# Optimization experiments

Measured on AMD Instinct MI355X. Metric: run time of the kernel, lower is better.

## Reference

```python
import jax, jax.numpy as jnp
import numpy as np

EPS = 1e-3  # keras LayerNormalization default epsilon


def layer_norm(x, gamma, beta):
    mu = jnp.mean(x, axis=-1, keepdims=True)
    var = jnp.var(x, axis=-1, keepdims=True)
    return (x - mu) * jax.lax.rsqrt(var + EPS) * gamma + beta


def setup_inputs() -> dict:
    key = jax.random.key(0)
    ks = jax.random.split(key, 16)
    B, S, D = 8, 2048, 1024          # batch, seq, input_size
    P = 2 * D                        # up-projection dim (proj_factor=2)
    H = 1024                         # hidden = head_size(64) * num_heads(16)
    s = 0.02
    inp = {
        "x": jax.random.normal(ks[0], (B, S, D), jnp.float32),
        "ln1_g": jnp.ones((D,), jnp.float32),
        "ln1_b": jnp.zeros((D,), jnp.float32),
        "W_up": jax.random.normal(ks[1], (D, P), jnp.float32) * s,
        "b_up": jnp.zeros((P,), jnp.float32),
        "W_adj": jax.random.normal(ks[2], (P, H), jnp.float32) * s,
        "b_adj": jnp.zeros((H,), jnp.float32),
        "W_q": jax.random.normal(ks[3], (H, H), jnp.float32) * s,
        "b_q": jnp.zeros((H,), jnp.float32),
        "W_k": jax.random.normal(ks[4], (H, H), jnp.float32) * s,
        "b_k": jnp.zeros((H,), jnp.float32),
        "W_v": jax.random.normal(ks[5], (H, H), jnp.float32) * s,
        "b_v": jnp.zeros((H,), jnp.float32),
        "W_i": jax.random.normal(ks[6], (H, H), jnp.float32) * s,
        "b_i": jnp.zeros((H,), jnp.float32),
        "W_f": jax.random.normal(ks[7], (H, H), jnp.float32) * s,
        "b_f": jnp.zeros((H,), jnp.float32),
        "W_o": jax.random.normal(ks[8], (H, H), jnp.float32) * s,
        "b_o": jnp.zeros((H,), jnp.float32),
        "ln2_g": jnp.ones((H,), jnp.float32),
        "ln2_b": jnpos if False else jnp.zeros((H,), jnp.float32),
        "W_down": jax.random.normal(ks[9], (H, D), jnp.float32) * s,
        "b_down": jnp.zeros((D,), jnp.float32),
    }
    return inp


def reference(x, ln1_g, ln1_b, W_up, b_up, W_adj, b_adj,
              W_q, b_q, W_k, b_k, W_v, b_v,
              W_i, b_i, W_f, b_f, W_o, b_o,
              ln2_g, ln2_b, W_down, b_down):
    head_size = 64
    x_norm = layer_norm(x, ln1_g, ln1_b)
    x_up = x_norm @ W_up + b_up                      # [B,S,2D]
    x_adj = x_up @ W_adj + b_adj                     # [B,S,H]
    # BlockDiagonal layers: each block is a Dense over the FULL input,
    # concatenated -> equivalent to one [H,H] matmul with concatenated weights.
    q = x_adj @ W_q + b_q
    k = (x_adj @ W_k + b_k) / (head_size ** 0.5)
    v = x_adj @ W_v + b_v
    i_t = x_adj @ W_i + b_i
    f_t = x_adj @ W_f + b_f
    o = jax.nn.sigmoid(x_adj @ W_o + b_o)
    m_t = jnp.maximum(f_t, i_t)
    f = jnp.exp(f_t - m_t)                           # (i = exp(i_t - m_t) unused downstream)
    c_t = f * v * k
    h_t = o * (c_t * q) / jnp.maximum(jnp.abs(k * q), 1.0)
    out = layer_norm(h_t, ln2_g, ln2_b) * jax.nn.sigmoid(x_adj)
    out = out @ W_down + b_down
    return out + x
```

## Files before the change

kernel.cpp:

```cpp
#include <hip/hip_runtime.h>


typedef unsigned short u16;
typedef __attribute__((ext_vector_type(4))) unsigned short u16x4;
typedef __attribute__((ext_vector_type(8))) __bf16 bf16x8;
typedef __attribute__((ext_vector_type(4))) float f32x4;

__device__ __forceinline__ float bf2f(u16 u) {
    union { unsigned int i; float f; } c; c.i = ((unsigned int)u) << 16; return c.f;
}
__device__ __forceinline__ u16 f2bf(float f) {
    union { float f; unsigned int i; } c; c.f = f;
    unsigned int lsb = (c.i >> 16) & 1u;
    c.i += 0x7fffu + lsb;
    return (u16)(c.i >> 16);
}
__device__ __forceinline__ float sigmoidf(float z) {
    return 1.0f / (1.0f + __expf(-z));
}

#define GLDS16(gp, lp)                                                        \
    __builtin_amdgcn_global_load_lds(                                         \
        (__attribute__((address_space(1))) void*)(void*)(gp),                 \
        (__attribute__((address_space(3))) void*)(lp), 16, 0, 0)

#define BM 128
#define BN 128
#define BK 32

template <int MODE>
__global__ __launch_bounds__(256) void gemm_bt(
    const u16* __restrict__ A, const u16* __restrict__ Bt,
    const float* __restrict__ bias, const float* __restrict__ resid,
    void* __restrict__ out, int M, int N, int K, float scale)
{
    __shared__ __align__(16) u16 As[2 * BM * BK];
    __shared__ __align__(16) u16 Bs[2 * BN * BK];

    const int tid  = threadIdx.x;
    const int lane = tid & 63;
    const int wave = tid >> 6;
    const int l15  = lane & 15;
    const int quad = lane >> 4;

    const long bm = (long)blockIdx.y * BM;
    const long bn = (long)blockIdx.x * BN;
    const int  wm = (wave >> 1) * 64;
    const int  wn = (wave & 1) * 64;

    f32x4 acc[4][4] = {};

    const int  r0 = tid >> 2;
    const int  ck = (((tid & 3) ^ ((tid >> 3) & 3)) * 8);
    const u16* ga0 = A  + (bm + r0) * (long)K + ck;
    const u16* gb0 = Bt + (bn + r0) * (long)K + ck;
    const int  ldst = wave * 512;

    auto stage = [&](int t_, int b_) {
        const long kof = (long)t_ * BK;
        u16* dA = &As[b_ * (BM * BK) + ldst];
        u16* dB = &Bs[b_ * (BN * BK) + ldst];
        GLDS16(ga0 + kof, dA);
        GLDS16(ga0 + kof + 64 * (long)K, dA + 2048);
        GLDS16(gb0 + kof, dB);
        GLDS16(gb0 + kof + 64 * (long)K, dB + 2048);
    };

    const int q8s = (quad ^ ((l15 >> 1) & 3)) * 8;
    const int nk  = K / BK;

    stage(0, 0);
    stage(1, 1);

    for (int t = 0; t < nk; ++t) {
        const int cur = t & 1;
        if (t + 1 < nk) asm volatile("s_waitcnt vmcnt(4)" ::: "memory");
        else            asm volatile("s_waitcnt vmcnt(0)" ::: "memory");
        __builtin_amdgcn_s_barrier();

        bf16x8 af[4], bfr[4];
#pragma unroll
        for (int t4 = 0; t4 < 4; ++t4) {
            af[t4]  = *(const bf16x8*)&As[cur * (BM * BK) + (wm + t4 * 16 + l15) * BK + q8s];
            bfr[t4] = *(const bf16x8*)&Bs[cur * (BN * BK) + (wn + t4 * 16 + l15) * BK + q8s];
        }
        asm volatile("s_waitcnt lgkmcnt(0)" ::: "memory");
        __builtin_amdgcn_s_barrier();
        if (t + 2 < nk) stage(t + 2, cur);

#pragma unroll
        for (int mt = 0; mt < 4; ++mt)
#pragma unroll
            for (int nt = 0; nt < 4; ++nt)
                acc[mt][nt] = __builtin_amdgcn_mfma_f32_16x16x32_bf16(
                    af[mt], bfr[nt], acc[mt][nt], 0, 0, 0);
    }

#pragma unroll
    for (int nt = 0; nt < 4; ++nt) {
        const long n  = bn + wn + nt * 16 + l15;
        const float bv = bias[n];
#pragma unroll
        for (int mt = 0; mt < 4; ++mt) {
            const long m0 = bm + wm + mt * 16 + quad * 4;
#pragma unroll
            for (int r = 0; r < 4; ++r) {
                const long idx = (m0 + r) * N + n;
                const float val = (acc[mt][nt][r] + bv) * scale;
                if (MODE == 0) ((u16*)out)[idx] = f2bf(val);
                else           ((float*)out)[idx] = val + resid[idx];
            }
        }
    }
}

__global__ __launch_bounds__(256) void gemm_gates(
    const u16* __restrict__ A, const u16* __restrict__ Wcat,
    const float* __restrict__ bq_, const float* __restrict__ bk_,
    const float* __restrict__ bv_, const float* __restrict__ bi_,
    const float* __restrict__ bf_, const float* __restrict__ bo_,
    u16* __restrict__ ht, int M, int N, int K)
{
    __shared__ __align__(16) u16 As[2 * 128 * 64];
    __shared__ __align__(16) u16 Bs[2 * 6 * 32 * 64];

    const int tid  = threadIdx.x;
    const int lane = tid & 63;
    const int wave = tid >> 6;
    const int l15  = lane & 15;
    const int quad = lane >> 4;

    const long bm = (long)blockIdx.y * 128;
    const long bn = (long)blockIdx.x * 32;

    f32x4 acc[6][4] = {};

    const int  rr = lane >> 3;
    const int  ck = (((lane & 7) ^ rr) * 8);

    const u16* gaj[4];
    int lAo[4];
#pragma unroll
    for (int j = 0; j < 4; ++j) {
        const int c = wave * 4 + j;
        gaj[j] = A + (bm + c * 8 + rr) * (long)K + ck;
        lAo[j] = c * 512;
    }
    const u16* gbj[6];
    int lBo[6];
#pragma unroll
    for (int j = 0; j < 6; ++j) {
        const int c = wave * 6 + j;
        const int g = c >> 2;
        const int r = (c & 3) * 8 + rr;
        gbj[j] = Wcat + ((long)g * 1024 + bn + r) * (long)K + ck;
        lBo[j] = c * 512;
    }

    auto stage = [&](int t_, int b_) {
        const long kof = (long)t_ * 64;
#pragma unroll
        for (int j = 0; j < 4; ++j)
            GLDS16(gaj[j] + kof, &As[b_ * 8192 + lAo[j]]);
#pragma unroll
        for (int j = 0; j < 6; ++j)
            GLDS16(gbj[j] + kof, &Bs[b_ * 12288 + lBo[j]]);
    };

    const int mh = (wave >> 1) * 64;
    const int nb = (wave & 1) * 16;
    const int l7 = l15 & 7;
    const int nk = K >> 6;

    stage(0, 0);
    stage(1, 1);

    for (int t = 0; t < nk; ++t) {
        const int cur = t & 1;
        if (t + 1 < nk) asm volatile("s_waitcnt vmcnt(10)" ::: "memory");
        else            asm volatile("s_waitcnt vmcnt(0)"  ::: "memory");
        __builtin_amdgcn_s_barrier();

        const int ab = cur * 8192;
        const int bb = cur * 12288;

        {
            const int so = (quad ^ l7) * 8;
            bf16x8 af[4];
#pragma unroll
            for (int t4 = 0; t4 < 4; ++t4)
                af[t4] = *(const bf16x8*)&As[ab + (mh + t4 * 16 + l15) * 64 + so];
#pragma unroll
            for (int g = 0; g < 6; ++g) {
                const bf16x8 bfrag =
                    *(const bf16x8*)&Bs[bb + (g * 32 + nb + l15) * 64 + so];
#pragma unroll
                for (int t4 = 0; t4 < 4; ++t4)
                    acc[g][t4] = __builtin_amdgcn_mfma_f32_16x16x32_bf16(
                        af[t4], bfrag, acc[g][t4], 0, 0, 0);
            }
        }
        bf16x8 af1[4], bf1[6];
        {
            const int so = ((4 + quad) ^ l7) * 8;
#pragma unroll
            for (int t4 = 0; t4 < 4; ++t4)
                af1[t4] = *(const bf16x8*)&As[ab + (mh + t4 * 16 + l15) * 64 + so];
#pragma unroll
            for (int g = 0; g < 6; ++g)
                bf1[g] = *(const bf16x8*)&Bs[bb + (g * 32 + nb + l15) * 64 + so];
        }
        asm volatile("s_waitcnt lgkmcnt(0)" ::: "memory");
        __builtin_amdgcn_s_barrier();
        if (t + 2 < nk) stage(t + 2, cur);

#pragma unroll
        for (int g = 0; g < 6; ++g)
#pragma unroll
            for (int t4 = 0; t4 < 4; ++t4)
                acc[g][t4] = __builtin_amdgcn_mfma_f32_16x16x32_bf16(
                    af1[t4], bf1[g], acc[g][t4], 0, 0, 0);
    }

    const long n = bn + nb + l15;
    const float bqn = bq_[n], bkn = bk_[n], bvn = bv_[n];
    const float bin = bi_[n], bfn = bf_[n], bon = bo_[n];
#pragma unroll
    for (int t = 0; t < 4; ++t) {
        const long m0 = bm + mh + t * 16 + quad * 4;
#pragma unroll
        for (int r = 0; r < 4; ++r) {
            const float qf = acc[0][t][r] + bqn;
            const float kf = (acc[1][t][r] + bkn) * 0.125f;
            const float vf = acc[2][t][r] + bvn;
            const float fi = acc[3][t][r] + bin;
            const float ff = acc[4][t][r] + bfn;
            const float osig = sigmoidf(acc[5][t][r] + bon);
            const float mx = fmaxf(ff, fi);
            const float fe = __expf(ff - mx);
            const float ct = fe * vf * kf;
            const float h  = osig * (ct * qf) / fmaxf(fabsf(kf * qf), 1.0f);
            ht[(m0 + r) * N + n] = f2bf(h);
        }
    }
}

__global__ __launch_bounds__(256) void ln_in_kernel(
    const float* __restrict__ x, const float* __restrict__ g,
    const float* __restrict__ b, u16* __restrict__ xn)
{
    const long row = blockIdx.x;
    const int  tid = threadIdx.x;
    const float4 v = ((const float4*)(x + row * 1024))[tid];
    float s  = v.x + v.y + v.z + v.w;
    float s2 = v.x * v.x + v.y * v.y + v.z * v.z + v.w * v.w;
#pragma unroll
    for (int off = 32; off > 0; off >>= 1) {
        s  += __shfl_down(s, off);
        s2 += __shfl_down(s2, off);
    }
    __shared__ float red[8];
    const int wave = tid >> 6;
    if ((tid & 63) == 0) { red[wave] = s; red[4 + wave] = s2; }
    __syncthreads();
    if (tid == 0) {
        const float S  = red[0] + red[1] + red[2] + red[3];
        const float S2 = red[4] + red[5] + red[6] + red[7];
        const float mu = S * (1.0f / 1024.0f);
        const float var = S2 * (1.0f / 1024.0f) - mu * mu;
        red[0] = mu; red[1] = rsqrtf(var + 1e-3f);
    }
    __syncthreads();
    const float mu = red[0], rstd = red[1];
    const int c = tid * 4;
    u16x4 o;
    o.x = f2bf((v.x - mu) * rstd * g[c + 0] + b[c + 0]);
    o.y = f2bf((v.y - mu) * rstd * g[c + 1] + b[c + 1]);
    o.z = f2bf((v.z - mu) * rstd * g[c + 2] + b[c + 2]);
    o.w = f2bf((v.w - mu) * rstd * g[c + 3] + b[c + 3]);
    *(u16x4*)(xn + row * 1024 + c) = o;
}

__global__ __launch_bounds__(256) void convT_kernel(
    const float* __restrict__ W, u16* __restrict__ Wt, int K, int N)
{
    __shared__ float t[32][33];
    const int tx = threadIdx.x & 31;
    const int ty = threadIdx.x >> 5;
    const long bn = (long)blockIdx.x * 32;
    const long bk = (long)blockIdx.y * 32;
#pragma unroll
    for (int j = 0; j < 4; ++j)
        t[ty + j * 8][tx] = W[(bk + ty + j * 8) * N + bn + tx];
    __syncthreads();
#pragma unroll
    for (int j = 0; j < 4; ++j)
        Wt[(bn + ty + j * 8) * K + bk + tx] = f2bf(t[tx][ty + j * 8]);
}

__global__ __launch_bounds__(256) void ln2_kernel(
    const u16* __restrict__ ht, const u16* __restrict__ xadj,
    const float* __restrict__ g2, const float* __restrict__ b2,
    u16* __restrict__ y)
{
    const long base = (long)blockIdx.x * 1024;
    const int  tid = threadIdx.x;
    const int  c = tid * 4;
    const u16x4 hv = *(const u16x4*)&ht[base + c];
    const u16x4 xv = *(const u16x4*)&xadj[base + c];

    float h[4];
    float s = 0.0f, s2 = 0.0f;
#pragma unroll
    for (int j = 0; j < 4; ++j) {
        h[j] = bf2f(hv[j]);
        s += h[j]; s2 += h[j] * h[j];
    }
#pragma unroll
    for (int off = 32; off > 0; off >>= 1) {
        s  += __shfl_down(s, off);
        s2 += __shfl_down(s2, off);
    }
    __shared__ float red[8];
    const int wave = tid >> 6;
    if ((tid & 63) == 0) { red[wave] = s; red[4 + wave] = s2; }
    __syncthreads();
    if (tid == 0) {
        const float S  = red[0] + red[1] + red[2] + red[3];
        const float S2 = red[4] + red[5] + red[6] + red[7];
        const float mu = S * (1.0f / 1024.0f);
        const float var = S2 * (1.0f / 1024.0f) - mu * mu;
        red[0] = mu; red[1] = rsqrtf(var + 1e-3f);
    }
    __syncthreads();
    const float mu = red[0], rstd = red[1];
    u16x4 o;
#pragma unroll
    for (int j = 0; j < 4; ++j)
        o[j] = f2bf(((h[j] - mu) * rstd * g2[c + j] + b2[c + j]) * sigmoidf(bf2f(xv[j])));
    *(u16x4*)&y[base + c] = o;
}

extern "C" void kernel_launch(void* const* d_in, const int* in_sizes, int n_in,
                              void* d_out, int out_size, void* d_ws, size_t ws_size,
                              hipStream_t stream)
{
    const float* x    = (const float*)d_in[0];
    const float* g1   = (const float*)d_in[1];
    const float* b1   = (const float*)d_in[2];
    const float* Wup  = (const float*)d_in[3];
    const float* bup  = (const float*)d_in[4];
    const float* Wadj = (const float*)d_in[5];
    const float* badj = (const float*)d_in[6];
    const float* Wq = (const float*)d_in[7];   const float* bq = (const float*)d_in[8];
    const float* Wk = (const float*)d_in[9];   const float* bk = (const float*)d_in[10];
    const float* Wv = (const float*)d_in[11];  const float* bv = (const float*)d_in[12];
    const float* Wi = (const float*)d_in[13];  const float* bi = (const float*)d_in[14];
    const float* Wf = (const float*)d_in[15];  const float* bf = (const float*)d_in[16];
    const float* Wo = (const float*)d_in[17];  const float* bo = (const float*)d_in[18];
    const float* g2 = (const float*)d_in[19];  const float* b2 = (const float*)d_in[20];
    const float* Wdn = (const float*)d_in[21]; const float* bdn = (const float*)d_in[22];

    const int M = 8 * 2048;
    const int D = 1024, P = 2048, H = 1024;

    char* ws = (char*)d_ws;
    const size_t MB = 1024 * 1024;
    u16* xn    = (u16*)(ws + 0);
    u16* xup   = (u16*)(ws + 32 * MB);
    u16* xadj  = (u16*)(ws + 96 * MB);
    u16* htb   = (u16*)(ws + 0);
    u16* yb    = (u16*)(ws + 0);
    u16* WupT  = (u16*)(ws + 128 * MB);
    u16* WadjT = (u16*)(ws + 132 * MB);
    u16* Wcat  = (u16*)(ws + 136 * MB);
    u16* WdnT  = (u16*)(ws + 148 * MB);

    ln_in_kernel<<<M, 256, 0, stream>>>(x, g1, b1, xn);

    convT_kernel<<<dim3(P / 32, D / 32), 256, 0, stream>>>(Wup,  WupT,  D, P);
    convT_kernel<<<dim3(H / 32, P / 32), 256, 0, stream>>>(Wadj, WadjT, P, H);
    convT_kernel<<<dim3(H / 32, H / 32), 256, 0, stream>>>(Wq, Wcat + 0 * H * H, H, H);
    convT_kernel<<<dim3(H / 32, H / 32), 256, 0, stream>>>(Wk, Wcat + 1 * H * H, H, H);
    convT_kernel<<<dim3(H / 32, H / 32), 256, 0, stream>>>(Wv, Wcat + 2 * H * H, H, H);
    convT_kernel<<<dim3(H / 32, H / 32), 256, 0, stream>>>(Wi, Wcat + 3 * H * H, H, H);
    convT_kernel<<<dim3(H / 32, H / 32), 256, 0, stream>>>(Wf, Wcat + 4 * H * H, H, H);
    convT_kernel<<<dim3(H / 32, H / 32), 256, 0, stream>>>(Wo, Wcat + 5 * H * H, H, H);
    convT_kernel<<<dim3(D / 32, H / 32), 256, 0, stream>>>(Wdn, WdnT, H, D);

    gemm_bt<0><<<dim3(P / BN, M / BM), 256, 0, stream>>>(xn,  WupT,  bup,  nullptr, xup,  M, P, D, 1.0f);
    gemm_bt<0><<<dim3(H / BN, M / BM), 256, 0, stream>>>(xup, WadjT, badj, nullptr, xadj, M, H, P, 1.0f);

    gemm_gates<<<dim3(H / 32, M / 128), 256, 0, stream>>>(
        xadj, Wcat, bq, bk, bv, bi, bf, bo, htb, M, H, H);

    ln2_kernel<<<M, 256, 0, stream>>>(htb, xadj, g2, b2, yb);

    gemm_bt<1><<<dim3(D / BN, M / BM), 256, 0, stream>>>(yb, WdnT, bdn, x, (float*)d_out, M, D, H, 1.0f);
}
```

Baseline: 662.4 us.

## Fold up-projection and adjust GEMMs into one combined weight matrix

```diff
diff --git a/kernel.cpp b/kernel.cpp
--- a/kernel.cpp
+++ b/kernel.cpp
@@ -3,6 +3,7 @@
 
 typedef unsigned short u16;
 typedef __attribute__((ext_vector_type(4))) unsigned short u16x4;
+typedef __attribute__((ext_vector_type(8))) unsigned short u16x8;
 typedef __attribute__((ext_vector_type(8))) __bf16 bf16x8;
 typedef __attribute__((ext_vector_type(4))) float f32x4;
 
@@ -99,7 +100,7 @@
 #pragma unroll
     for (int nt = 0; nt < 4; ++nt) {
         const long n  = bn + wn + nt * 16 + l15;
-        const float bv = bias[n];
+        const float bv = (MODE == 2) ? 0.0f : bias[n];
 #pragma unroll
         for (int mt = 0; mt < 4; ++mt) {
             const long m0 = bm + wm + mt * 16 + quad * 4;
@@ -107,8 +108,8 @@
             for (int r = 0; r < 4; ++r) {
                 const long idx = (m0 + r) * N + n;
                 const float val = (acc[mt][nt][r] + bv) * scale;
-                if (MODE == 0) ((u16*)out)[idx] = f2bf(val);
-                else           ((float*)out)[idx] = val + resid[idx];
+                if (MODE == 1) ((float*)out)[idx] = val + resid[idx];
+                else           ((u16*)out)[idx] = f2bf(val);
             }
         }
     }
@@ -296,6 +297,37 @@
 #pragma unroll
     for (int j = 0; j < 4; ++j)
         Wt[(bn + ty + j * 8) * K + bk + tx] = f2bf(t[tx][ty + j * 8]);
+}
+
+__global__ __launch_bounds__(256) void convB_kernel(
+    const float* __restrict__ W, u16* __restrict__ Wb)
+{
+    const long i = ((long)blockIdx.x * 256 + threadIdx.x) * 4;
+    const float4 v = *(const float4*)(W + i);
+    u16x4 o;
+    o.x = f2bf(v.x); o.y = f2bf(v.y); o.z = f2bf(v.z); o.w = f2bf(v.w);
+    *(u16x4*)(Wb + i) = o;
+}
+
+__global__ __launch_bounds__(256) void bcomb_kernel(
+    const u16* __restrict__ WadjT, const float* __restrict__ bup,
+    const float* __restrict__ badj, float* __restrict__ bcomb)
+{
+    const long h = blockIdx.x;
+    const int  tid = threadIdx.x;
+    const int  p = tid * 8;
+    const u16x8 w = *(const u16x8*)&WadjT[h * 2048 + p];
+    float s = 0.0f;
+#pragma unroll
+    for (int j = 0; j < 8; ++j) s += bf2f(w[j]) * bup[p + j];
+#pragma unroll
+    for (int off = 32; off > 0; off >>= 1) s += __shfl_down(s, off);
+    __shared__ float red[4];
+    const int wave = tid >> 6;
+    if ((tid & 63) == 0) red[wave] = s;
+    __syncthreads();
+    if (tid == 0)
+        bcomb[h] = red[0] + red[1] + red[2] + red[3] + badj[h];
 }
 
 __global__ __launch_bounds__(256) void ln2_kernel(
@@ -366,19 +398,20 @@
 
     char* ws = (char*)d_ws;
     const size_t MB = 1024 * 1024;
-    u16* xn    = (u16*)(ws + 0);
-    u16* xup   = (u16*)(ws + 32 * MB);
-    u16* xadj  = (u16*)(ws + 96 * MB);
-    u16* htb   = (u16*)(ws + 0);
-    u16* yb    = (u16*)(ws + 0);
-    u16* WupT  = (u16*)(ws + 128 * MB);
-    u16* WadjT = (u16*)(ws + 132 * MB);
-    u16* Wcat  = (u16*)(ws + 136 * MB);
-    u16* WdnT  = (u16*)(ws + 148 * MB);
+    u16* xn     = (u16*)(ws + 0);
+    u16* htb    = (u16*)(ws + 0);
+    u16* yb     = (u16*)(ws + 0);
+    u16* WcombT = (u16*)(ws + 32 * MB);
+    float* bcomb = (float*)(ws + 36 * MB);
+    u16* xadj   = (u16*)(ws + 96 * MB);
+    u16* Wup_bf = (u16*)(ws + 128 * MB);
+    u16* WadjT  = (u16*)(ws + 132 * MB);
+    u16* Wcat   = (u16*)(ws + 136 * MB);
+    u16* WdnT   = (u16*)(ws + 148 * MB);
 
     ln_in_kernel<<<M, 256, 0, stream>>>(x, g1, b1, xn);
 
-    convT_kernel<<<dim3(P / 32, D / 32), 256, 0, stream>>>(Wup,  WupT,  D, P);
+    convB_kernel<<<(D * P) / (256 * 4), 256, 0, stream>>>(Wup, Wup_bf);
     convT_kernel<<<dim3(H / 32, P / 32), 256, 0, stream>>>(Wadj, WadjT, P, H);
     convT_kernel<<<dim3(H / 32, H / 32), 256, 0, stream>>>(Wq, Wcat + 0 * H * H, H, H);
     convT_kernel<<<dim3(H / 32, H / 32), 256, 0, stream>>>(Wk, Wcat + 1 * H * H, H, H);
@@ -387,9 +420,13 @@
     convT_kernel<<<dim3(H / 32, H / 32), 256, 0, stream>>>(Wf, Wcat + 4 * H * H, H, H);
     convT_kernel<<<dim3(H / 32, H / 32), 256, 0, stream>>>(Wo, Wcat + 5 * H * H, H, H);
     convT_kernel<<<dim3(D / 32, H / 32), 256, 0, stream>>>(Wdn, WdnT, H, D);
-
-    gemm_bt<0><<<dim3(P / BN, M / BM), 256, 0, stream>>>(xn,  WupT,  bup,  nullptr, xup,  M, P, D, 1.0f);
-    gemm_bt<0><<<dim3(H / BN, M / BM), 256, 0, stream>>>(xup, WadjT, badj, nullptr, xadj, M, H, P, 1.0f);
+    bcomb_kernel<<<H, 256, 0, stream>>>(WadjT, bup, badj, bcomb);
+
+    gemm_bt<2><<<dim3(D / BN, H / BM), 256, 0, stream>>>(
+        WadjT, Wup_bf, nullptr, nullptr, WcombT, H, D, P, 1.0f);
+
+    gemm_bt<0><<<dim3(H / BN, M / BM), 256, 0, stream>>>(
+        xn, WcombT, bcomb, nullptr, xadj, M, H, D, 1.0f);
 
     gemm_gates<<<dim3(H / 32, M / 128), 256, 0, stream>>>(
         xadj, Wcat, bq, bk, bv, bi, bf, bo, htb, M, H, H);
```

Result: faster. 569.1 us (-14.1%).
